# Optimization experiments

Hardware: AMD Instinct MI355X
Metric: run time of the kernel (lower is better)

## Reference

```python
import jax, jax.numpy as jnp
import numpy as np

def setup_inputs() -> dict:
    key = jax.random.key(0)
    kq, kk, kv = jax.random.split(key, 3)
    B, H, N, D = 2, 12, 4096, 64
    Q = jax.random.normal(kq, (B, H, N, D), dtype=jnp.float32)
    K = jax.random.normal(kk, (B, H, N, D), dtype=jnp.float32)
    V = jax.random.normal(kv, (B, H, N, D), dtype=jnp.float32)
    mask = jnp.ones((B, N), dtype=jnp.float32)
    return {"Q": Q, "K": K, "V": V, "mask": mask}

def reference(Q, K, V, mask):
    # Q, K, V: [B, H, N, D]; mask: [B, N]
    N = Q.shape[2]
    scale = 1.0 / jnp.sqrt(jnp.sqrt(jnp.float32(N)))  # N^(-1/4)
    m = mask[:, None, :, None]                         # [B,1,N,1]
    Qf = (jax.nn.elu(Q) + 1.0) * scale                 # feature map on queries
    Kf = (jax.nn.elu(K) + 1.0) * m * scale             # feature map + mask on keys
    Vm = V * m
    # linear attention: Q (K^T V), contracting over sequence first -> [B,H,D,D]
    KtV = jnp.einsum('bhnd,bhne->bhde', Kf, Vm)
    X = jnp.einsum('bhnd,bhde->bhne', Qf, KtV)
    return X
```

## Files before the change

kernel.cpp:

```cpp
#include <hip/hip_runtime.h>
#include <hip/hip_bf16.h>
#include <math.h>


#define BH_TOT 24
#define NROWS 4096
#define DD 64
#define SLABS 16

typedef __attribute__((ext_vector_type(8))) short bf16x8;
typedef __attribute__((ext_vector_type(4))) float f32x4;

__device__ __forceinline__ float elu1(float x) {
    return x > 0.0f ? x + 1.0f : __expf(x);
}
__device__ __forceinline__ short f2bf(float x) {
    __hip_bfloat16 h = __float2bfloat16(x);
    return *reinterpret_cast<short*>(&h);
}

__global__ __launch_bounds__(256) void la_pass1(
        const float* __restrict__ K, const float* __restrict__ V,
        const float* __restrict__ mask, float* __restrict__ partial,
        float scale) {
    const int bh   = blockIdx.x;
    const int slab = blockIdx.y;
    const int wave = threadIdx.x >> 6;
    const int lane = threadIdx.x & 63;
    const int g = lane >> 4, rg = g * 8, cl = lane & 15;

    const float* __restrict__ Kp = K + (size_t)bh * NROWS * DD;
    const float* __restrict__ Vp = V + (size_t)bh * NROWS * DD;
    const float* __restrict__ mp = mask + (size_t)(bh / 12) * NROWS;

    const int n0 = (slab * 4 + wave) * 64;

    float mrow[2][8], kr[2][8][4], vr[2][8][4];
#pragma unroll
    for (int c = 0; c < 2; ++c) {
        const int nb = n0 + c * 32 + rg;
        const float* kb = Kp + (size_t)nb * DD + cl;
        const float* vb = Vp + (size_t)nb * DD + cl;
#pragma unroll
        for (int jj = 0; jj < 8; ++jj) {
            mrow[c][jj] = mp[nb + jj];
#pragma unroll
            for (int i = 0; i < 4; ++i) {
                kr[c][jj][i] = kb[jj * DD + i * 16];
                vr[c][jj][i] = vb[jj * DD + i * 16];
            }
        }
    }

    f32x4 acc[4][4];
#pragma unroll
    for (int je = 0; je < 4; ++je)
#pragma unroll
        for (int id = 0; id < 4; ++id) acc[je][id] = (f32x4)0.0f;

#pragma unroll
    for (int c = 0; c < 2; ++c) {
        bf16x8 af[4], bv[4];
#pragma unroll
        for (int i = 0; i < 4; ++i)
#pragma unroll
            for (int jj = 0; jj < 8; ++jj) {
                af[i][jj] = f2bf(elu1(kr[c][jj][i]) * (mrow[c][jj] * scale));
                bv[i][jj] = f2bf(vr[c][jj][i] * mrow[c][jj]);
            }
#pragma unroll
        for (int je = 0; je < 4; ++je)
#pragma unroll
            for (int id = 0; id < 4; ++id)
                acc[je][id] = __builtin_amdgcn_mfma_f32_16x16x32_bf16(
                                  bv[je], af[id], acc[je][id], 0, 0, 0);
    }

    __shared__ f32x4 red[2][16][64];
    if (wave >= 2) {
#pragma unroll
        for (int je = 0; je < 4; ++je)
#pragma unroll
            for (int id = 0; id < 4; ++id)
                red[wave - 2][je * 4 + id][lane] = acc[je][id];
    }
    __syncthreads();
    if (wave < 2) {
#pragma unroll
        for (int je = 0; je < 4; ++je)
#pragma unroll
            for (int id = 0; id < 4; ++id)
                acc[je][id] += red[wave][je * 4 + id][lane];
    }
    __syncthreads();
    if (wave == 1) {
#pragma unroll
        for (int je = 0; je < 4; ++je)
#pragma unroll
            for (int id = 0; id < 4; ++id)
                red[0][je * 4 + id][lane] = acc[je][id];
    }
    __syncthreads();
    if (wave == 0) {
        f32x4* out = (f32x4*)partial + ((size_t)bh * SLABS + slab) * 1024;
#pragma unroll
        for (int je = 0; je < 4; ++je)
#pragma unroll
            for (int id = 0; id < 4; ++id)
                out[(je * 4 + id) * 64 + lane]
                    = acc[je][id] + red[0][je * 4 + id][lane];
    }
}

__global__ __launch_bounds__(256) void la_pass2(
        const float* __restrict__ partial, __hip_bfloat16* __restrict__ ktvT) {
    const int bh  = blockIdx.x;
    const int pos = blockIdx.y * 256 + threadIdx.x;
    const f32x4* base = (const f32x4*)partial + (size_t)bh * SLABS * 1024 + pos;
    f32x4 s = (f32x4)0.0f;
#pragma unroll 8
    for (int w = 0; w < SLABS; ++w)
        s += base[(size_t)w * 1024];
    const int frag = pos >> 6, ln = pos & 63;
    const int e0 = 16 * (frag >> 2) + 4 * (ln >> 4);
    const int d  = 16 * (frag & 3) + (ln & 15);
    __hip_bfloat16* ko = ktvT + (size_t)bh * DD * DD;
#pragma unroll
    for (int r = 0; r < 4; ++r)
        ko[(size_t)(e0 + r) * DD + d] = __float2bfloat16(s[r]);
}

__global__ __launch_bounds__(256) void la_pass3(
        const float* __restrict__ Q, const __hip_bfloat16* __restrict__ ktvT,
        float* __restrict__ X, float scale) {
    const int bh   = blockIdx.x;
    const int wave = threadIdx.x >> 6;
    const int lane = threadIdx.x & 63;
    const int n0   = blockIdx.y * 128 + wave * 32;
    const int g = lane >> 4, rg = g * 8, cl = lane & 15;

    bf16x8 afr[4][2];
#pragma unroll
    for (int i = 0; i < 4; ++i)
#pragma unroll
        for (int c2 = 0; c2 < 2; ++c2)
            afr[i][c2] = *reinterpret_cast<const bf16x8*>(
                ktvT + (size_t)bh * DD * DD + (size_t)(16 * i + cl) * DD + 32 * c2 + rg);

    const float* Qp = Q + (size_t)bh * NROWS * DD;
    bf16x8 bfr[2][2];
#pragma unroll
    for (int t = 0; t < 2; ++t)
#pragma unroll
        for (int c2 = 0; c2 < 2; ++c2) {
            const float* qp = Qp + (size_t)(n0 + 16 * t + cl) * DD + 32 * c2 + rg;
            float4 q0 = ((const float4*)qp)[0];
            float4 q1 = ((const float4*)qp)[1];
            bf16x8 a;
            a[0] = f2bf(elu1(q0.x) * scale); a[1] = f2bf(elu1(q0.y) * scale);
            a[2] = f2bf(elu1(q0.z) * scale); a[3] = f2bf(elu1(q0.w) * scale);
            a[4] = f2bf(elu1(q1.x) * scale); a[5] = f2bf(elu1(q1.y) * scale);
            a[6] = f2bf(elu1(q1.z) * scale); a[7] = f2bf(elu1(q1.w) * scale);
            bfr[t][c2] = a;
        }

    f32x4 acc[4][2];
#pragma unroll
    for (int i = 0; i < 4; ++i)
#pragma unroll
        for (int t = 0; t < 2; ++t) acc[i][t] = (f32x4)0.0f;

#pragma unroll
    for (int i = 0; i < 4; ++i)
#pragma unroll
        for (int t = 0; t < 2; ++t) {
            acc[i][t] = __builtin_amdgcn_mfma_f32_16x16x32_bf16(
                            afr[i][0], bfr[t][0], acc[i][t], 0, 0, 0);
            acc[i][t] = __builtin_amdgcn_mfma_f32_16x16x32_bf16(
                            afr[i][1], bfr[t][1], acc[i][t], 0, 0, 0);
        }

    float* Xp = X + (size_t)bh * NROWS * DD;
#pragma unroll
    for (int i = 0; i < 4; ++i)
#pragma unroll
        for (int t = 0; t < 2; ++t) {
            float4 v = make_float4(acc[i][t][0], acc[i][t][1],
                                   acc[i][t][2], acc[i][t][3]);
            *reinterpret_cast<float4*>(
                Xp + (size_t)(n0 + 16 * t + cl) * DD + 16 * i + 4 * g) = v;
        }
}

extern "C" void kernel_launch(void* const* d_in, const int* in_sizes, int n_in,
                              void* d_out, int out_size, void* d_ws, size_t ws_size,
                              hipStream_t stream) {
    const float* Q    = (const float*)d_in[0];
    const float* K    = (const float*)d_in[1];
    const float* V    = (const float*)d_in[2];
    const float* mask = (const float*)d_in[3];
    float* X = (float*)d_out;

    const float scale = 0.125f;

    float* partial = (float*)d_ws;
    __hip_bfloat16* ktvT =
        (__hip_bfloat16*)((char*)d_ws + (size_t)BH_TOT * SLABS * DD * DD * 4);

    la_pass1<<<dim3(BH_TOT, SLABS), 256, 0, stream>>>(K, V, mask, partial, scale);
    la_pass2<<<dim3(BH_TOT, 4), 256, 0, stream>>>(partial, ktvT);
    la_pass3<<<dim3(BH_TOT, 32), 256, 0, stream>>>(Q, ktvT, X, scale);
}
```

Measured before the change: 30.51 us.

## Fuse slab reduction into output pass with XCD-aware block mapping

Removes the separate reduction kernel: each output block now sums the per-slab K^T V partials itself and stores the bf16 result in shared memory before the MFMA stage. Blocks are remapped so that all blocks for a given batch-head land on the same XCD, so the repeated partial reads can hit L2. This saves a kernel launch and the global round trip of the reduced matrix. In exchange, every one of the 32 blocks per head redundantly re-reads all 16 slabs of partials.

```diff
diff --git a/kernel.cpp b/kernel.cpp
--- a/kernel.cpp
+++ b/kernel.cpp
@@ -112,32 +112,42 @@
     }
 }
 
-__global__ __launch_bounds__(256) void la_pass2(
-        const float* __restrict__ partial, __hip_bfloat16* __restrict__ ktvT) {
-    const int bh  = blockIdx.x;
-    const int pos = blockIdx.y * 256 + threadIdx.x;
-    const f32x4* base = (const f32x4*)partial + (size_t)bh * SLABS * 1024 + pos;
-    f32x4 s = (f32x4)0.0f;
-#pragma unroll 8
-    for (int w = 0; w < SLABS; ++w)
-        s += base[(size_t)w * 1024];
-    const int frag = pos >> 6, ln = pos & 63;
-    const int e0 = 16 * (frag >> 2) + 4 * (ln >> 4);
-    const int d  = 16 * (frag & 3) + (ln & 15);
-    __hip_bfloat16* ko = ktvT + (size_t)bh * DD * DD;
-#pragma unroll
-    for (int r = 0; r < 4; ++r)
-        ko[(size_t)(e0 + r) * DD + d] = __float2bfloat16(s[r]);
-}
-
 __global__ __launch_bounds__(256) void la_pass3(
-        const float* __restrict__ Q, const __hip_bfloat16* __restrict__ ktvT,
+        const float* __restrict__ Q, const float* __restrict__ partial,
         float* __restrict__ X, float scale) {
-    const int bh   = blockIdx.x;
+    const int bid   = blockIdx.x;
+    const int xcd   = bid & 7;
+    const int q     = bid >> 3;
+    const int hi    = q % 3;
+    const int qslab = q / 3;
+    const int bh    = xcd + 8 * hi;
+
     const int wave = threadIdx.x >> 6;
     const int lane = threadIdx.x & 63;
-    const int n0   = blockIdx.y * 128 + wave * 32;
     const int g = lane >> 4, rg = g * 8, cl = lane & 15;
+
+    __shared__ unsigned short ktv[DD][72];
+
+    {
+        const f32x4* base = (const f32x4*)partial + (size_t)bh * SLABS * 1024;
+#pragma unroll
+        for (int p = 0; p < 4; ++p) {
+            const int pos = threadIdx.x + p * 256;
+            f32x4 s = (f32x4)0.0f;
+#pragma unroll
+            for (int w = 0; w < SLABS; ++w)
+                s += base[(size_t)w * 1024 + pos];
+            const int frag = pos >> 6, ln = pos & 63;
+            const int e0 = 16 * (frag >> 2) + 4 * (ln >> 4);
+            const int d  = 16 * (frag & 3) + (ln & 15);
+#pragma unroll
+            for (int r = 0; r < 4; ++r)
+                ktv[e0 + r][d] = (unsigned short)f2bf(s[r]);
+        }
+    }
+    __syncthreads();
+
+    const int n0 = qslab * 128 + wave * 32;
 
     bf16x8 afr[4][2];
 #pragma unroll
@@ -145,7 +155,7 @@
 #pragma unroll
         for (int c2 = 0; c2 < 2; ++c2)
             afr[i][c2] = *reinterpret_cast<const bf16x8*>(
-                ktvT + (size_t)bh * DD * DD + (size_t)(16 * i + cl) * DD + 32 * c2 + rg);
+                &ktv[16 * i + cl][32 * c2 + rg]);
 
     const float* Qp = Q + (size_t)bh * NROWS * DD;
     bf16x8 bfr[2][2];
@@ -204,10 +214,7 @@
     const float scale = 0.125f;
 
     float* partial = (float*)d_ws;
-    __hip_bfloat16* ktvT =
-        (__hip_bfloat16*)((char*)d_ws + (size_t)BH_TOT * SLABS * DD * DD * 4);
 
     la_pass1<<<dim3(BH_TOT, SLABS), 256, 0, stream>>>(K, V, mask, partial, scale);
-    la_pass2<<<dim3(BH_TOT, 4), 256, 0, stream>>>(partial, ktvT);
-    la_pass3<<<dim3(BH_TOT, 32), 256, 0, stream>>>(Q, ktvT, X, scale);
-}
+    la_pass3<<<768, 256, 0, stream>>>(Q, partial, X, scale);
+}
```

Result: slower. 32.42 us (+6.3%).
